# Kernel tuning notes

Hardware: AMD Instinct MI355X
Metric: run time of the kernel (lower is better)

The kernel has to match this reference:

```python
import jax, jax.numpy as jnp
import numpy as np

B, C, H, W, NCH = 2, 256, 48, 48, 12


def setup_inputs() -> dict:
    key = jax.random.key(0)
    k1, k2, k3, k4, k5 = jax.random.split(key, 5)
    gray_feature = jax.random.normal(k1, (B, C, H, W), jnp.float32)
    rgb_feature = jax.random.normal(k2, (B, C, H, W), jnp.float32)
    rgb_image = jax.random.uniform(k3, (B, 3, H, W), jnp.float32)
    # one-hot segmentation labels: random class id per pixel in [0, NCH)
    gcls = jax.random.randint(k4, (B, H, W), 0, NCH)
    rcls = jax.random.randint(k5, (B, H, W), 0, NCH)
    gray_label = jax.nn.one_hot(gcls, NCH, axis=1, dtype=jnp.float32)
    rgb_label = jax.nn.one_hot(rcls, NCH, axis=1, dtype=jnp.float32)
    return dict(gray_feature=gray_feature, rgb_feature=rgb_feature,
                rgb_image=rgb_image, gray_label=gray_label, rgb_label=rgb_label)


def _masked_normalize(feat, maskf):
    # feat: [b,c,N], maskf: [b,N] in {0,1}. Subtract per-channel masked mean,
    # then divide each masked pixel's feature vector by its channel-norm.
    cnt = maskf.sum(-1)                                            # [b]
    mean = jnp.einsum('bcn,bn->bc', feat, maskf) / jnp.maximum(cnt, 1.0)[:, None]
    bar = (feat - mean[:, :, None]) * maskf[:, None, :]            # zero outside mask
    norm = jnp.sqrt(jnp.sum(bar * bar, axis=1))                    # [b,N]
    unit = bar / jnp.where(norm > 0, norm, 1.0)[:, None, :]
    return unit, cnt


def reference(gray_feature, rgb_feature, rgb_image, gray_label, rgb_label):
    b, c, h, w = gray_feature.shape
    N = h * w
    gf = gray_feature.reshape(b, c, N)
    rf = rgb_feature.reshape(b, c, N)
    img = rgb_image.reshape(b, 3, N)
    gms = gray_label.reshape(b, -1, N) > 0.5   # [b,NCH,N] bool
    rms = rgb_label.reshape(b, -1, N) > 0.5
    canvas = -jnp.ones((b, 3, N), gray_feature.dtype)
    NEG = jnp.asarray(-1e30, gray_feature.dtype)
    for k in range(1, 12):  # classes 1..11, matching the torch loop
        gm = gms[:, k]                                     # [b,N]
        rm = rms[:, k]
        gmf = gm.astype(gf.dtype)
        rmf = rm.astype(rf.dtype)
        gn, cg = _masked_normalize(gf, gmf)                # [b,c,N]
        rn, cr = _masked_normalize(rf, rmf)
        # normalized correlation between gray and rgb masked pixels
        corr = jnp.einsum('bci,bcj->bij', gn, rn)          # [b,N,N]
        logits = jnp.where(rm[:, None, :], corr, NEG)      # softmax over rgb-mask pixels
        sm = jax.nn.softmax(logits, axis=-1)
        out = jnp.einsum('bij,bcj->bci', sm, img)          # [b,3,N]
        # skip condition from torch: needs >=2 pixels on each side
        valid = (cg > 1) & (cr > 1)                        # [b]
        write = gm & valid[:, None]                        # [b,N]
        canvas = jnp.where(write[:, None, :], out, canvas)
    return canvas.reshape(b, 3, h, w)
```

## Files before the change

kernel.cpp:

```cpp
#include <hip/hip_runtime.h>
#include <math.h>

#define BN 2
#define CC 256
#define NN 2304
#define KK 12
#define MC 320
#define QT 8
#define KTL 256
#define KCH 32
#define BPAD 260
#define APAD 10

#define OFF_CNT_G   0
#define OFF_CNT_R   32
#define OFF_IDX_G   64
#define OFF_CPS_G   (OFF_IDX_G + BN * KK * MC)
#define OFF_CPS_R   (OFF_CPS_G + BN * NN)
#define OFF_MSUM_G  (OFF_CPS_R + BN * NN)
#define OFF_MSUM_R  (OFF_MSUM_G + BN * KK * CC)
#define OFF_IMGC    (OFF_MSUM_R + BN * KK * CC)
#define OFF_INV_G   (OFF_IMGC + BN * KK * 3 * MC)
#define OFF_INV_R   (OFF_INV_G + BN * KK * MC)
#define OFF_UCG     (OFF_INV_R + BN * KK * MC)
#define OFF_UCR     (OFF_UCG + BN * KK * MC * CC)

__global__ __launch_bounds__(256) void prep_mean_kernel(
        const float* __restrict__ gf, const float* __restrict__ rf,
        const float* __restrict__ img, const float* __restrict__ gl,
        const float* __restrict__ rl, float* __restrict__ out,
        int* cnt_g, int* cnt_r, int* idx_g, int* cps_g, int* cps_r,
        float* imgc, float* inv_g, float* inv_r,
        float* msum_g, float* msum_r) {
    __shared__ int wcnt[4];
    __shared__ float wsum[4][4][KK];
    int bid = blockIdx.x, tid = threadIdx.x;
    int lane = tid & 63, wid = tid >> 6;

    if (bid < 48) {
        int type = bid / (BN * KK);
        int rem = bid % (BN * KK);
        int b = rem / KK, k = rem % KK;
        const float* lp = (type ? rl : gl) + ((size_t)(b * KK + k)) * NN;
        int* cps = type ? cps_r : cps_g;
        int* cnt = type ? cnt_r : cnt_g;
        int base = 0;
        for (int c0 = 0; c0 < NN; c0 += 256) {
            int i = c0 + tid;
            bool p = lp[i] > 0.5f;
            unsigned long long m = __ballot(p);
            int rank = __popcll(m & ((1ull << lane) - 1));
            if (lane == 0) wcnt[wid] = __popcll(m);
            __syncthreads();
            int pre = 0;
            for (int w = 0; w < wid; ++w) pre += wcnt[w];
            int tot = wcnt[0] + wcnt[1] + wcnt[2] + wcnt[3];
            if (p) {
                int pos = base + pre + rank;
                cps[b * NN + i] = (k << 16) | pos;
                if (pos < MC) {
                    if (type) {
                        for (int ch = 0; ch < 3; ++ch)
                            imgc[((b * KK + k) * 3 + ch) * MC + pos] =
                                img[((size_t)(b * 3 + ch)) * NN + i];
                    } else {
                        idx_g[(b * KK + k) * MC + pos] = i;
                    }
                }
            }
            base += tot;
            __syncthreads();
        }
        if (tid == 0) cnt[b * KK + k] = base;
        int start = base < MC ? base : MC;
        for (int pos = start + tid; pos < MC; pos += 256) {
            if (type) {
                for (int ch = 0; ch < 3; ++ch)
                    imgc[((b * KK + k) * 3 + ch) * MC + pos] = 0.f;
            } else {
                idx_g[(b * KK + k) * MC + pos] = 0;
            }
        }
        float* invc = type ? inv_r : inv_g;
        for (int pos = tid; pos < MC; pos += 256)
            invc[(b * KK + k) * MC + pos] = 0.f;
    } else {
        int u = bid - 48;
        if (u < 54) out[u * 256 + tid] = -1.0f;
        int type = u >> 7;
        int rem = u & 127;
        int b = rem >> 6, cg = rem & 63;
        const float* fb = (type ? rf : gf) + ((size_t)(b * CC + cg * 4)) * NN;
        const float* lab = (type ? rl : gl) + ((size_t)b) * KK * NN;
        float* msum = type ? msum_r : msum_g;

        float acc[4][KK];
        #pragma unroll
        for (int c = 0; c < 4; ++c)
            #pragma unroll
            for (int kk = 0; kk < KK; ++kk) acc[c][kk] = 0.f;
        for (int i = tid; i < NN; i += 256) {
            float lv[KK];
            #pragma unroll
            for (int kk = 0; kk < KK; ++kk) lv[kk] = lab[(size_t)kk * NN + i];
            #pragma unroll
            for (int c = 0; c < 4; ++c) {
                float v = fb[(size_t)c * NN + i];
                #pragma unroll
                for (int kk = 0; kk < KK; ++kk) acc[c][kk] += lv[kk] * v;
            }
        }
        #pragma unroll
        for (int c = 0; c < 4; ++c)
            #pragma unroll
            for (int kk = 0; kk < KK; ++kk) {
                #pragma unroll
                for (int o = 32; o; o >>= 1)
                    acc[c][kk] += __shfl_xor(acc[c][kk], o, 64);
            }
        if (lane == 0) {
            #pragma unroll
            for (int c = 0; c < 4; ++c)
                #pragma unroll
                for (int kk = 0; kk < KK; ++kk) wsum[wid][c][kk] = acc[c][kk];
        }
        __syncthreads();
        if (tid < 48) {
            int c = tid / KK, kk = tid % KK;
            float s = wsum[0][c][kk] + wsum[1][c][kk] + wsum[2][c][kk] + wsum[3][c][kk];
            msum[(b * KK + kk) * CC + cg * 4 + c] = s;
        }
    }
}

__global__ __launch_bounds__(256) void center_kernel(
        const float* __restrict__ gf, const float* __restrict__ rf,
        const int* __restrict__ cps_g, const int* __restrict__ cps_r,
        const int* __restrict__ cnt_g, const int* __restrict__ cnt_r,
        const float* __restrict__ msum_g, const float* __restrict__ msum_r,
        float* ucg, float* ucr, float* inv_g, float* inv_r) {
    const int PCH = NN / 32;
    int blk = blockIdx.x;
    int type = blk / (BN * PCH);
    int rem = blk % (BN * PCH);
    int b = rem / PCH, chunk = rem % PCH;
    int i0 = chunk * 32;
    const float* f = type ? rf : gf;
    const int* cps = type ? cps_r : cps_g;
    const int* cnt = type ? cnt_r : cnt_g;
    const float* msum = type ? msum_r : msum_g;
    float* uc = type ? ucr : ucg;
    float* invc = type ? inv_r : inv_g;

    __shared__ float lmean[KK * 257];
    __shared__ float tile[64 * 33];

    int tid = threadIdx.x;
    for (int x = tid; x < KK * CC; x += 256) {
        int k = x >> 8, c = x & 255;
        float cn = fmaxf((float)cnt[b * KK + k], 1.f);
        lmean[k * 257 + c] = msum[(b * KK + k) * CC + c] / cn;
    }
    int p = tid >> 3, q = tid & 7;
    int pl = tid & 31, cb = tid >> 5;
    int kcpos = cps[b * NN + i0 + p];
    int kc = kcpos >> 16, pos = kcpos & 0xFFFF;
    bool wr = pos < MC;
    float ss = 0.f;
    float* ub = uc + ((size_t)((b * KK + kc) * MC + (wr ? pos : MC - 1))) * CC;
    for (int cc = 0; cc < 4; ++cc) {
        __syncthreads();
        for (int j = 0; j < 8; ++j) {
            int c = cb * 8 + j;
            tile[c * 33 + pl] = f[((size_t)(b * CC + cc * 64 + c)) * NN + i0 + pl];
        }
        __syncthreads();
        #pragma unroll
        for (int h = 0; h < 2; ++h) {
            int c0 = q * 8 + h * 4;
            float4 v;
            v.x = tile[(c0 + 0) * 33 + p] - lmean[kc * 257 + cc * 64 + c0 + 0];
            v.y = tile[(c0 + 1) * 33 + p] - lmean[kc * 257 + cc * 64 + c0 + 1];
            v.z = tile[(c0 + 2) * 33 + p] - lmean[kc * 257 + cc * 64 + c0 + 2];
            v.w = tile[(c0 + 3) * 33 + p] - lmean[kc * 257 + cc * 64 + c0 + 3];
            ss += v.x * v.x + v.y * v.y + v.z * v.z + v.w * v.w;
            if (wr) *(float4*)&ub[cc * 64 + c0] = v;
        }
    }
    ss += __shfl_xor(ss, 1, 64);
    ss += __shfl_xor(ss, 2, 64);
    ss += __shfl_xor(ss, 4, 64);
    if (q == 0 && wr)
        invc[(b * KK + kc) * MC + pos] = (ss > 0.f) ? rsqrtf(ss) : 1.0f;
}

__global__ __launch_bounds__(256) void corr_out_kernel(
        const int* __restrict__ cnt_g, const int* __restrict__ cnt_r,
        const int* __restrict__ idx_g,
        const float* __restrict__ ucg, const float* __restrict__ ucr,
        const float* __restrict__ inv_g, const float* __restrict__ inv_r,
        const float* __restrict__ imgc, float* __restrict__ out) {
    const int TNQ = MC / QT;
    int tq = blockIdx.x % TNQ;
    int k = (blockIdx.x / TNQ) % KK;
    int b = blockIdx.x / (TNQ * KK);
    if (k == 0) return;
    int bk = b * KK + k;
    int cg_ = cnt_g[bk], cr_ = cnt_r[bk];
    if (cg_ <= 1 || cr_ <= 1) return;
    int Mg = min(cg_, MC), Mr = min(cr_, MC);
    int q0 = tq * QT;
    if (q0 >= Mg) return;

    __shared__ float Af[CC * APAD];
    __shared__ float Bs[KCH * BPAD];

    int tid = threadIdx.x;
    {
        int r = tid >> 5, c32 = tid & 31;
        int rowi = q0 + r; if (rowi > MC - 1) rowi = MC - 1;
        const float* rowA = ucg + ((size_t)(bk * MC + rowi)) * CC;
        float4 v0 = *(const float4*)&rowA[c32 * 8];
        float4 v1 = *(const float4*)&rowA[c32 * 8 + 4];
        Af[(c32 * 8 + 0) * APAD + r] = v0.x;
        Af[(c32 * 8 + 1) * APAD + r] = v0.y;
        Af[(c32 * 8 + 2) * APAD + r] = v0.z;
        Af[(c32 * 8 + 3) * APAD + r] = v0.w;
        Af[(c32 * 8 + 4) * APAD + r] = v1.x;
        Af[(c32 * 8 + 5) * APAD + r] = v1.y;
        Af[(c32 * 8 + 6) * APAD + r] = v1.z;
        Af[(c32 * 8 + 7) * APAD + r] = v1.w;
    }

    int ty = tid >> 6;
    int lane = tid & 63;
    int r0 = q0 + 2 * ty;
    int r0c = (r0 > MC - 1) ? MC - 1 : r0;
    int r1c = (r0 + 1 > MC - 1) ? MC - 1 : r0 + 1;
    float invi0 = inv_g[bk * MC + r0c];
    float invi1 = inv_g[bk * MC + r1c];
    const float* im0 = imgc + (bk * 3 + 0) * MC;
    const float* im1 = imgc + (bk * 3 + 1) * MC;
    const float* im2 = imgc + (bk * 3 + 2) * MC;
    const float* ivr = inv_r + bk * MC;
    float s[2] = {0.f, 0.f}, p0[2] = {0.f, 0.f}, p1[2] = {0.f, 0.f}, p2[2] = {0.f, 0.f};

    for (int k0 = 0; k0 < Mr; k0 += KTL) {
        float acc[2][4];
        #pragma unroll
        for (int x = 0; x < 2; ++x)
            #pragma unroll
            for (int y = 0; y < 4; ++y) acc[x][y] = 0.f;

        for (int kcc = 0; kcc < CC; kcc += KCH) {
            __syncthreads();
            {
                int cj = tid & 7;
                int colg = tid >> 3;
                #pragma unroll
                for (int p8 = 0; p8 < 8; ++p8) {
                    int col = colg + p8 * 32;
                    int colr = k0 + col; if (colr > MC - 1) colr = MC - 1;
                    float4 vb = *(const float4*)(ucr +
                        ((size_t)(bk * MC + colr)) * CC + kcc + cj * 4);
                    Bs[(cj * 4 + 0) * BPAD + col] = vb.x;
                    Bs[(cj * 4 + 1) * BPAD + col] = vb.y;
                    Bs[(cj * 4 + 2) * BPAD + col] = vb.z;
                    Bs[(cj * 4 + 3) * BPAD + col] = vb.w;
                }
            }
            __syncthreads();
            #pragma unroll
            for (int kk = 0; kk < KCH; ++kk) {
                float2 av = *(const float2*)&Af[(kcc + kk) * APAD + 2 * ty];
                float4 bv = *(const float4*)&Bs[kk * BPAD + lane * 4];
                acc[0][0] += av.x * bv.x; acc[0][1] += av.x * bv.y;
                acc[0][2] += av.x * bv.z; acc[0][3] += av.x * bv.w;
                acc[1][0] += av.y * bv.x; acc[1][1] += av.y * bv.y;
                acc[1][2] += av.y * bv.z; acc[1][3] += av.y * bv.w;
            }
        }
        int kbase = k0 + lane * 4; if (kbase > MC - 4) kbase = MC - 4;
        float4 w0 = *(const float4*)&im0[kbase];
        float4 w1 = *(const float4*)&im1[kbase];
        float4 w2 = *(const float4*)&im2[kbase];
        float4 vj = *(const float4*)&ivr[kbase];
        float wj0[4] = {w0.x, w0.y, w0.z, w0.w};
        float wj1[4] = {w1.x, w1.y, w1.z, w1.w};
        float wj2[4] = {w2.x, w2.y, w2.z, w2.w};
        float vjj[4] = {vj.x, vj.y, vj.z, vj.w};
        #pragma unroll
        for (int y = 0; y < 4; ++y) {
            int col = k0 + lane * 4 + y;
            bool ok = col < Mr;
            float e0 = ok ? __expf(acc[0][y] * invi0 * vjj[y]) : 0.f;
            float e1 = ok ? __expf(acc[1][y] * invi1 * vjj[y]) : 0.f;
            s[0] += e0; p0[0] += e0 * wj0[y]; p1[0] += e0 * wj1[y]; p2[0] += e0 * wj2[y];
            s[1] += e1; p0[1] += e1 * wj0[y]; p1[1] += e1 * wj1[y]; p2[1] += e1 * wj2[y];
        }
    }
    #pragma unroll
    for (int o = 1; o <= 32; o <<= 1) {
        #pragma unroll
        for (int x = 0; x < 2; ++x) {
            s[x]  += __shfl_xor(s[x],  o, 64);
            p0[x] += __shfl_xor(p0[x], o, 64);
            p1[x] += __shfl_xor(p1[x], o, 64);
            p2[x] += __shfl_xor(p2[x], o, 64);
        }
    }
    if (lane == 0) {
        #pragma unroll
        for (int x = 0; x < 2; ++x) {
            int row = q0 + 2 * ty + x;
            if (row < Mg) {
                int gi = idx_g[bk * MC + row];
                float inv = 1.0f / s[x];
                out[((size_t)(b * 3 + 0)) * NN + gi] = p0[x] * inv;
                out[((size_t)(b * 3 + 1)) * NN + gi] = p1[x] * inv;
                out[((size_t)(b * 3 + 2)) * NN + gi] = p2[x] * inv;
            }
        }
    }
}

extern "C" void kernel_launch(void* const* d_in, const int* in_sizes, int n_in,
                              void* d_out, int out_size, void* d_ws, size_t ws_size,
                              hipStream_t stream) {
    const float* gf  = (const float*)d_in[0];
    const float* rf  = (const float*)d_in[1];
    const float* img = (const float*)d_in[2];
    const float* gl  = (const float*)d_in[3];
    const float* rl  = (const float*)d_in[4];
    float* out = (float*)d_out;
    float* ws = (float*)d_ws;

    int*   cnt_g  = (int*)(ws + OFF_CNT_G);
    int*   cnt_r  = (int*)(ws + OFF_CNT_R);
    int*   idx_g  = (int*)(ws + OFF_IDX_G);
    int*   cps_g  = (int*)(ws + OFF_CPS_G);
    int*   cps_r  = (int*)(ws + OFF_CPS_R);
    float* msum_g = ws + OFF_MSUM_G;
    float* msum_r = ws + OFF_MSUM_R;
    float* imgc   = ws + OFF_IMGC;
    float* inv_g  = ws + OFF_INV_G;
    float* inv_r  = ws + OFF_INV_R;
    float* ucg    = ws + OFF_UCG;
    float* ucr    = ws + OFF_UCR;

    prep_mean_kernel<<<48 + 2 * BN * (CC / 4), 256, 0, stream>>>(
        gf, rf, img, gl, rl, out, cnt_g, cnt_r, idx_g, cps_g, cps_r,
        imgc, inv_g, inv_r, msum_g, msum_r);
    center_kernel<<<2 * BN * (NN / 32), 256, 0, stream>>>(
        gf, rf, cps_g, cps_r, cnt_g, cnt_r, msum_g, msum_r,
        ucg, ucr, inv_g, inv_r);
    corr_out_kernel<<<BN * KK * (MC / QT), 256, 0, stream>>>(
        cnt_g, cnt_r, idx_g, ucg, ucr, inv_g, inv_r, imgc, out);
}
```

Baseline: 114.5 us.

## Double rows per correlation block, skip class-0 blocks, remap block order, skip padded loads

Raises the number of gray rows per block from 8 to 16 and the block size to 512 threads, so each staged tile of rgb features in shared memory is reused by twice as many rows. The grid is rebuilt so only the 11 active classes get blocks, and block ids are permuted with a stride of 8 to spread work across the chip. Loads of rgb columns past the rounded-up valid count are skipped; columns left stale in shared memory are masked out of the softmax. The trade-offs are fewer blocks in flight, higher register and LDS pressure per block, and extra branching in the load loop.

```diff
diff --git a/kernel.cpp b/kernel.cpp
--- a/kernel.cpp
+++ b/kernel.cpp
@@ -6,11 +6,12 @@
 #define NN 2304
 #define KK 12
 #define MC 320
-#define QT 8
+#define QT 16
 #define KTL 256
 #define KCH 32
 #define BPAD 260
-#define APAD 10
+#define APAD 18
+#define KB_ACT 11
 
 #define OFF_CNT_G   0
 #define OFF_CNT_R   32
@@ -194,23 +195,27 @@
         invc[(b * KK + kc) * MC + pos] = (ss > 0.f) ? rsqrtf(ss) : 1.0f;
 }
 
-__global__ __launch_bounds__(256) void corr_out_kernel(
+__global__ __launch_bounds__(512) void corr_out_kernel(
         const int* __restrict__ cnt_g, const int* __restrict__ cnt_r,
         const int* __restrict__ idx_g,
         const float* __restrict__ ucg, const float* __restrict__ ucr,
         const float* __restrict__ inv_g, const float* __restrict__ inv_r,
         const float* __restrict__ imgc, float* __restrict__ out) {
     const int TNQ = MC / QT;
-    int tq = blockIdx.x % TNQ;
-    int k = (blockIdx.x / TNQ) % KK;
-    int b = blockIdx.x / (TNQ * KK);
-    if (k == 0) return;
+    const int NWG = BN * KB_ACT * TNQ;
+    int bid = blockIdx.x;
+    int x = (bid & 7) * (NWG / 8) + (bid >> 3);
+    int tq = x % TNQ;
+    int rest = x / TNQ;
+    int k = 1 + rest % KB_ACT;
+    int b = rest / KB_ACT;
     int bk = b * KK + k;
     int cg_ = cnt_g[bk], cr_ = cnt_r[bk];
     if (cg_ <= 1 || cr_ <= 1) return;
     int Mg = min(cg_, MC), Mr = min(cr_, MC);
     int q0 = tq * QT;
     if (q0 >= Mg) return;
+    int mrp = (Mr + 3) & ~3;
 
     __shared__ float Af[CC * APAD];
     __shared__ float Bs[KCH * BPAD];
@@ -232,9 +237,9 @@
         Af[(c32 * 8 + 7) * APAD + r] = v1.w;
     }
 
-    int ty = tid >> 6;
+    int wid = tid >> 6;
     int lane = tid & 63;
-    int r0 = q0 + 2 * ty;
+    int r0 = q0 + 2 * wid;
     int r0c = (r0 > MC - 1) ? MC - 1 : r0;
     int r1c = (r0 + 1 > MC - 1) ? MC - 1 : r0 + 1;
     float invi0 = inv_g[bk * MC + r0c];
@@ -248,9 +253,10 @@
     for (int k0 = 0; k0 < Mr; k0 += KTL) {
         float acc[2][4];
         #pragma unroll
-        for (int x = 0; x < 2; ++x)
-            #pragma unroll
-            for (int y = 0; y < 4; ++y) acc[x][y] = 0.f;
+        for (int xx = 0; xx < 2; ++xx)
+            #pragma unroll
+            for (int y = 0; y < 4; ++y) acc[xx][y] = 0.f;
+        int lim = mrp - k0;
 
         for (int kcc = 0; kcc < CC; kcc += KCH) {
             __syncthreads();
@@ -258,21 +264,23 @@
                 int cj = tid & 7;
                 int colg = tid >> 3;
                 #pragma unroll
-                for (int p8 = 0; p8 < 8; ++p8) {
-                    int col = colg + p8 * 32;
-                    int colr = k0 + col; if (colr > MC - 1) colr = MC - 1;
-                    float4 vb = *(const float4*)(ucr +
-                        ((size_t)(bk * MC + colr)) * CC + kcc + cj * 4);
-                    Bs[(cj * 4 + 0) * BPAD + col] = vb.x;
-                    Bs[(cj * 4 + 1) * BPAD + col] = vb.y;
-                    Bs[(cj * 4 + 2) * BPAD + col] = vb.z;
-                    Bs[(cj * 4 + 3) * BPAD + col] = vb.w;
+                for (int p8 = 0; p8 < 4; ++p8) {
+                    int col = colg + p8 * 64;
+                    if (col < lim) {
+                        int colr = k0 + col; if (colr > MC - 1) colr = MC - 1;
+                        float4 vb = *(const float4*)(ucr +
+                            ((size_t)(bk * MC + colr)) * CC + kcc + cj * 4);
+                        Bs[(cj * 4 + 0) * BPAD + col] = vb.x;
+                        Bs[(cj * 4 + 1) * BPAD + col] = vb.y;
+                        Bs[(cj * 4 + 2) * BPAD + col] = vb.z;
+                        Bs[(cj * 4 + 3) * BPAD + col] = vb.w;
+                    }
                 }
             }
             __syncthreads();
             #pragma unroll
             for (int kk = 0; kk < KCH; ++kk) {
-                float2 av = *(const float2*)&Af[(kcc + kk) * APAD + 2 * ty];
+                float2 av = *(const float2*)&Af[(kcc + kk) * APAD + 2 * wid];
                 float4 bv = *(const float4*)&Bs[kk * BPAD + lane * 4];
                 acc[0][0] += av.x * bv.x; acc[0][1] += av.x * bv.y;
                 acc[0][2] += av.x * bv.z; acc[0][3] += av.x * bv.w;
@@ -302,23 +310,23 @@
     #pragma unroll
     for (int o = 1; o <= 32; o <<= 1) {
         #pragma unroll
-        for (int x = 0; x < 2; ++x) {
-            s[x]  += __shfl_xor(s[x],  o, 64);
-            p0[x] += __shfl_xor(p0[x], o, 64);
-            p1[x] += __shfl_xor(p1[x], o, 64);
-            p2[x] += __shfl_xor(p2[x], o, 64);
+        for (int xx = 0; xx < 2; ++xx) {
+            s[xx]  += __shfl_xor(s[xx],  o, 64);
+            p0[xx] += __shfl_xor(p0[xx], o, 64);
+            p1[xx] += __shfl_xor(p1[xx], o, 64);
+            p2[xx] += __shfl_xor(p2[xx], o, 64);
         }
     }
     if (lane == 0) {
         #pragma unroll
-        for (int x = 0; x < 2; ++x) {
-            int row = q0 + 2 * ty + x;
+        for (int xx = 0; xx < 2; ++xx) {
+            int row = q0 + 2 * wid + xx;
             if (row < Mg) {
                 int gi = idx_g[bk * MC + row];
-                float inv = 1.0f / s[x];
-                out[((size_t)(b * 3 + 0)) * NN + gi] = p0[x] * inv;
-                out[((size_t)(b * 3 + 1)) * NN + gi] = p1[x] * inv;
-                out[((size_t)(b * 3 + 2)) * NN + gi] = p2[x] * inv;
+                float inv = 1.0f / s[xx];
+                out[((size_t)(b * 3 + 0)) * NN + gi] = p0[xx] * inv;
+                out[((size_t)(b * 3 + 1)) * NN + gi] = p1[xx] * inv;
+                out[((size_t)(b * 3 + 2)) * NN + gi] = p2[xx] * inv;
             }
         }
     }
@@ -354,6 +362,6 @@
     center_kernel<<<2 * BN * (NN / 32), 256, 0, stream>>>(
         gf, rf, cps_g, cps_r, cnt_g, cnt_r, msum_g, msum_r,
         ucg, ucr, inv_g, inv_r);
-    corr_out_kernel<<<BN * KK * (MC / QT), 256, 0, stream>>>(
+    corr_out_kernel<<<BN * KB_ACT * (MC / QT), 512, 0, stream>>>(
         cnt_g, cnt_r, idx_g, ucg, ucr, inv_g, inv_r, imgc, out);
 }
```

Result: no change. 113.8 us (-0.6%).
